# Kernel optimization log

Measured on AMD Instinct MI355X. Metric: run time of the kernel, lower is better.

Reference implementation:

```python
import jax, jax.numpy as jnp
import numpy as np

RATIO = 0.5
BN_EPS = 1e-5
L2_EPS = 1e-8


def setup_inputs() -> dict:
    key = jax.random.key(0)
    ks = jax.random.split(key, 8)
    B, L, D, E = 64, 577, 512, 1024
    H = E // 2  # MLP hidden = embed_dim // 2 = 512
    base_features = jax.random.normal(ks[0], (B, L, D), dtype=jnp.float32)
    atten = jax.random.uniform(ks[1], (B, L, L), dtype=jnp.float32)
    s_fc = 1.0 / np.sqrt(D)
    s_h = 1.0 / np.sqrt(H)
    return {
        "base_features": base_features,
        "atten": atten,
        "fc_w": jax.random.uniform(ks[2], (E, D), jnp.float32, -s_fc, s_fc),
        "fc_b": jax.random.uniform(ks[3], (E,), jnp.float32, -s_fc, s_fc),
        "mlp_w0": jax.random.uniform(ks[4], (H, D), jnp.float32, -s_fc, s_fc),
        "mlp_b0": jax.random.uniform(ks[5], (H,), jnp.float32, -s_fc, s_fc),
        "bn0_gamma": jnp.ones((H,), jnp.float32),
        "bn0_beta": jnp.zeros((H,), jnp.float32),
        "mlp_w1": jax.random.uniform(ks[6], (E, H), jnp.float32, -s_h, s_h),
        "mlp_b1": jax.random.uniform(ks[7], (E,), jnp.float32, -s_h, s_h),
    }


def _forward(base_features, atten, fc_w, fc_b, mlp_w0, mlp_b0,
             bn0_gamma, bn0_beta, mlp_w1, mlp_b1):
    B, L, D = base_features.shape
    k = int((L - 1) * RATIO)  # static: derived from shape

    # atten[:, :, 0] = -1; rank tokens by CLS-row attention atten[:, 0]
    scores = atten[:, 0].at[:, 0].set(-1.0)           # [B, L]
    idx = jax.lax.top_k(scores, k)[1]                 # [B, k]

    # gather selected tokens: [B, k, D]
    feats = jnp.take_along_axis(base_features, idx[:, :, None], axis=1)

    # l2norm over last dim (norm = sqrt(sum(x^2)) + eps, then divide)
    norm = jnp.sqrt(jnp.sum(feats * feats, axis=-1, keepdims=True)) + L2_EPS
    feats = feats / norm

    # MLP (num_layers=2): Linear -> BN(training-mode batch stats) -> ReLU -> Linear
    x = feats.reshape(B * k, D)
    h = x @ mlp_w0.T + mlp_b0                         # [B*k, H]
    mu = jnp.mean(h, axis=0)
    var = jnp.mean((h - mu) ** 2, axis=0)             # biased var, as torch BN
    h = jax.nn.relu(bn0_gamma * (h - mu) * jax.lax.rsqrt(var + BN_EPS) + bn0_beta)
    x_att = (h @ mlp_w1.T + mlp_b1).reshape(B, k, -1)  # [B, k, E]

    local = jnp.einsum('bkd,ed->bke', feats, fc_w) + fc_b + x_att

    # maxk_pool1d_var with k=1 and full lengths == max over sequence dim
    return jnp.max(local, axis=1).astype(jnp.float32)  # [B, E]


def reference(base_features, atten, fc_w, fc_b, mlp_w0, mlp_b0,
              bn0_gamma, bn0_beta, mlp_w1, mlp_b1):
    return _forward(base_features, atten, fc_w, fc_b, mlp_w0, mlp_b0,
                    bn0_gamma, bn0_beta, mlp_w1, mlp_b1)
```

## Files before the change

### kernel.cpp

```cpp
#include <hip/hip_runtime.h>
#include <math.h>

#define B_   64
#define L_   577
#define D_   512
#define E_   1024
#define H_   512
#define K_   288
#define N_   (B_ * K_)
#define KBIG 1024

typedef __attribute__((ext_vector_type(8))) __bf16 bf16x8;
typedef __attribute__((ext_vector_type(4))) float f32x4;
typedef __attribute__((ext_vector_type(4))) unsigned short ushort4v;

#define OFF_WBIG    0
#define OFF_W0B     (2097152)
#define OFF_BIASBIG (2097152 + 524288)
#define OFF_MUSIG   (OFF_BIASBIG + 4096)
#define OFF_IDX     (OFF_MUSIG + 4096)
#define OFF_PART    (OFF_IDX + 73728)
#define OFF_ABIG    (OFF_PART + 524288)
#define OFF_H       (OFF_ABIG + (size_t)N_ * KBIG * 2)
#define OFF_LOCAL   (OFF_H + (size_t)N_ * H_ * 4)

static __device__ __forceinline__ unsigned short f2bf(float f) {
  unsigned int u = __builtin_bit_cast(unsigned int, f);
  u = (u + 0x7fffu + ((u >> 16) & 1u)) >> 16;
  return (unsigned short)u;
}

#define GLOAD_LDS16(g, l)                                          \
  __builtin_amdgcn_global_load_lds(                                \
      (const __attribute__((address_space(1))) void*)(g),          \
      (__attribute__((address_space(3))) void*)(l), 16, 0, 0)

__global__ __launch_bounds__(256) void prep_kernel(
    const float* __restrict__ fc_w, const float* __restrict__ fc_b,
    const float* __restrict__ w0,   const float* __restrict__ w1,
    const float* __restrict__ b1,
    unsigned short* __restrict__ wbig, unsigned short* __restrict__ w0b,
    float* __restrict__ biasbig) {
  int gid = blockIdx.x * 256 + threadIdx.x;
  if (gid < 262144) {
    int e  = gid >> 8;
    int c4 = gid & 255;
    float4 v;
    if (c4 < 128) v = ((const float4*)(fc_w + e * D_))[c4];
    else          v = ((const float4*)(w1   + e * H_))[c4 - 128];
    ushort4v o = { f2bf(v.x), f2bf(v.y), f2bf(v.z), f2bf(v.w) };
    ((ushort4v*)wbig)[gid] = o;
    if (gid < E_) biasbig[gid] = fc_b[gid] + b1[gid];
  } else {
    int idx = gid - 262144;
    float4 v = ((const float4*)w0)[idx];
    ushort4v o = { f2bf(v.x), f2bf(v.y), f2bf(v.z), f2bf(v.w) };
    ((ushort4v*)w0b)[idx] = o;
  }
}

__global__ __launch_bounds__(256) void topk_kernel(
    const float* __restrict__ atten, int* __restrict__ idx) {
  __shared__ float s[L_];
  int b = blockIdx.x;
  const float* row = atten + (size_t)b * L_ * L_;
  for (int i = threadIdx.x; i < L_; i += 256) s[i] = (i == 0) ? -1.0f : row[i];
  __syncthreads();
  for (int i = threadIdx.x; i < L_; i += 256) {
    float si = s[i];
    int rank = 0;
    for (int j = 0; j < L_; ++j) {
      float sj = s[j];
      rank += (sj > si) || (sj == si && j < i);
    }
    if (rank < K_) idx[b * K_ + rank] = i;
  }
}

__global__ __launch_bounds__(128) void gather_norm_kernel(
    const float* __restrict__ base, const int* __restrict__ idx,
    unsigned short* __restrict__ abig) {
  int r = blockIdx.x;
  int b = r / K_;
  int tok = idx[r];
  const float* src = base + ((size_t)b * L_ + tok) * D_;
  float4 v = ((const float4*)src)[threadIdx.x];
  float ss = v.x * v.x + v.y * v.y + v.z * v.z + v.w * v.w;
  #pragma unroll
  for (int o = 32; o > 0; o >>= 1) ss += __shfl_down(ss, o, 64);
  __shared__ float wsum[2];
  if ((threadIdx.x & 63) == 0) wsum[threadIdx.x >> 6] = ss;
  __syncthreads();
  float total = wsum[0] + wsum[1];
  float inv = 1.0f / (sqrtf(total) + 1e-8f);
  ushort4v o4 = { f2bf(v.x * inv), f2bf(v.y * inv), f2bf(v.z * inv), f2bf(v.w * inv) };
  ((ushort4v*)(abig + (size_t)r * KBIG))[threadIdx.x] = o4;
}

__global__ __launch_bounds__(256) void gemm_mfma_kernel(
    const unsigned short* __restrict__ A, int lda,
    const unsigned short* __restrict__ W, int ldw,
    const float* __restrict__ bias,
    float* __restrict__ C, int ldc, int K) {
  __shared__ unsigned short As[128 * 32];
  __shared__ unsigned short Bs[128 * 32];
  const int tid  = threadIdx.x;
  const int wave = tid >> 6;
  const int lane = tid & 63;
  const int m0 = blockIdx.x * 128;
  const int n0 = blockIdx.y * 128;

  const int srow0 = 16 * wave + (lane >> 2);
  const int srow1 = srow0 + 64;
  const int scol  = (lane & 3) * 8;
  const unsigned short* ag0 = A + (size_t)(m0 + srow0) * lda + scol;
  const unsigned short* ag1 = A + (size_t)(m0 + srow1) * lda + scol;
  const unsigned short* wg0 = W + (size_t)(n0 + srow0) * ldw + scol;
  const unsigned short* wg1 = W + (size_t)(n0 + srow1) * ldw + scol;
  unsigned short* as_dst0 = &As[srow0 * 32 + scol];
  unsigned short* as_dst1 = &As[srow1 * 32 + scol];
  unsigned short* bs_dst0 = &Bs[srow0 * 32 + scol];
  unsigned short* bs_dst1 = &Bs[srow1 * 32 + scol];

  const int quad = lane >> 4;
  const int l15  = lane & 15;
  const int wm = (wave & 1) * 64;
  const int wn = (wave >> 1) * 64;

  f32x4 acc[4][4];
  #pragma unroll
  for (int i = 0; i < 4; ++i)
    #pragma unroll
    for (int j = 0; j < 4; ++j)
      acc[i][j] = (f32x4)(0.0f);

  for (int k0 = 0; k0 < K; k0 += 32) {
    GLOAD_LDS16(ag0 + k0, as_dst0);
    GLOAD_LDS16(ag1 + k0, as_dst1);
    GLOAD_LDS16(wg0 + k0, bs_dst0);
    GLOAD_LDS16(wg1 + k0, bs_dst1);
    __syncthreads();
    bf16x8 af[4], bfr[4];
    #pragma unroll
    for (int i = 0; i < 4; ++i)
      af[i] = *(const bf16x8*)&As[(wm + 16 * i + l15) * 32 + quad * 8];
    #pragma unroll
    for (int j = 0; j < 4; ++j)
      bfr[j] = *(const bf16x8*)&Bs[(wn + 16 * j + l15) * 32 + quad * 8];
    #pragma unroll
    for (int i = 0; i < 4; ++i)
      #pragma unroll
      for (int j = 0; j < 4; ++j)
        acc[i][j] = __builtin_amdgcn_mfma_f32_16x16x32_bf16(af[i], bfr[j], acc[i][j], 0, 0, 0);
    __syncthreads();
  }

  #pragma unroll
  for (int i = 0; i < 4; ++i) {
    int row_base = m0 + wm + 16 * i + quad * 4;
    #pragma unroll
    for (int j = 0; j < 4; ++j) {
      int col = n0 + wn + 16 * j + l15;
      float bb = bias[col];
      #pragma unroll
      for (int r = 0; r < 4; ++r)
        C[(size_t)(row_base + r) * ldc + col] = acc[i][j][r] + bb;
    }
  }
}

__global__ __launch_bounds__(256) void bn_stats1_kernel(
    const float* __restrict__ h, float* __restrict__ partial) {
  int blk = blockIdx.x;
  int t = threadIdx.x;
  int r0 = blk * 144;
  float s0 = 0.f, q0 = 0.f, s1 = 0.f, q1 = 0.f;
  for (int i = 0; i < 144; ++i) {
    const float* row = h + (size_t)(r0 + i) * H_;
    float a = row[t], b2 = row[t + 256];
    s0 += a; q0 += a * a; s1 += b2; q1 += b2 * b2;
  }
  partial[blk * 512 + t] = s0;
  partial[blk * 512 + t + 256] = s1;
  partial[65536 + blk * 512 + t] = q0;
  partial[65536 + blk * 512 + t + 256] = q1;
}

__global__ __launch_bounds__(256) void bn_stats2_kernel(
    const float* __restrict__ partial, float* __restrict__ musig) {
  int c = blockIdx.x * 256 + threadIdx.x;
  float S = 0.f, Q = 0.f;
  for (int i = 0; i < 128; ++i) {
    S += partial[i * 512 + c];
    Q += partial[65536 + i * 512 + c];
  }
  const float invN = 1.0f / (float)N_;
  float mu = S * invN;
  float var = Q * invN - mu * mu;
  musig[c] = mu;
  musig[512 + c] = rsqrtf(var + 1e-5f);
}

__global__ __launch_bounds__(256) void bn_apply_kernel(
    const float* __restrict__ h, unsigned short* __restrict__ abig,
    const float* __restrict__ musig,
    const float* __restrict__ gamma, const float* __restrict__ beta) {
  int gid = blockIdx.x * 256 + threadIdx.x;
  int r = gid >> 7;
  int c4 = gid & 127;
  int c = c4 * 4;
  float4 v = *((const float4*)(h + (size_t)r * H_) + c4);
  float vv[4] = {v.x, v.y, v.z, v.w};
  unsigned short o[4];
  #pragma unroll
  for (int j = 0; j < 4; ++j) {
    float x = (vv[j] - musig[c + j]) * musig[512 + c + j] * gamma[c + j] + beta[c + j];
    o[j] = f2bf(fmaxf(x, 0.0f));
  }
  ushort4v ov = { o[0], o[1], o[2], o[3] };
  *((ushort4v*)(abig + (size_t)r * KBIG + H_) + c4) = ov;
}

__global__ __launch_bounds__(256) void maxk_kernel(
    const float* __restrict__ local, float* __restrict__ out) {
  int gid = blockIdx.x * 256 + threadIdx.x;
  int b = gid >> 10, e = gid & 1023;
  const float* p = local + (size_t)b * K_ * KBIG + e;
  float m = -INFINITY;
  for (int j = 0; j < K_; ++j) m = fmaxf(m, p[(size_t)j * KBIG]);
  out[gid] = m;
}

extern "C" void kernel_launch(void* const* d_in, const int* in_sizes, int n_in,
                              void* d_out, int out_size, void* d_ws, size_t ws_size,
                              hipStream_t stream) {
  const float* base  = (const float*)d_in[0];
  const float* atten = (const float*)d_in[1];
  const float* fc_w  = (const float*)d_in[2];
  const float* fc_b  = (const float*)d_in[3];
  const float* w0    = (const float*)d_in[4];
  const float* b0    = (const float*)d_in[5];
  const float* gamma = (const float*)d_in[6];
  const float* beta  = (const float*)d_in[7];
  const float* w1    = (const float*)d_in[8];
  const float* b1    = (const float*)d_in[9];
  float* out = (float*)d_out;

  char* ws = (char*)d_ws;
  unsigned short* wbig    = (unsigned short*)(ws + OFF_WBIG);
  unsigned short* w0b     = (unsigned short*)(ws + OFF_W0B);
  float*          biasbig = (float*)(ws + OFF_BIASBIG);
  float*          musig   = (float*)(ws + OFF_MUSIG);
  int*            idx     = (int*)  (ws + OFF_IDX);
  float*          partial = (float*)(ws + OFF_PART);
  unsigned short* abig    = (unsigned short*)(ws + OFF_ABIG);
  float*          h       = (float*)(ws + OFF_H);
  float*          local   = (float*)(ws + OFF_LOCAL);

  prep_kernel<<<1280, 256, 0, stream>>>(fc_w, fc_b, w0, w1, b1, wbig, w0b, biasbig);
  topk_kernel<<<B_, 256, 0, stream>>>(atten, idx);
  gather_norm_kernel<<<N_, 128, 0, stream>>>(base, idx, abig);
  {
    dim3 grid(N_ / 128, H_ / 128);
    gemm_mfma_kernel<<<grid, 256, 0, stream>>>(abig, KBIG, w0b, D_, b0, h, H_, D_);
  }
  bn_stats1_kernel<<<128, 256, 0, stream>>>(h, partial);
  bn_stats2_kernel<<<2, 256, 0, stream>>>(partial, musig);
  bn_apply_kernel<<<(N_ * 128) / 256, 256, 0, stream>>>(h, abig, musig, gamma, beta);
  {
    dim3 grid(N_ / 128, E_ / 128);
    gemm_mfma_kernel<<<grid, 256, 0, stream>>>(abig, KBIG, wbig, KBIG, biasbig,
                                               local, KBIG, KBIG);
  }
  maxk_kernel<<<(B_ * E_) / 256, 256, 0, stream>>>(local, out);
}
```

Measured before the change: 355.9 us.

## Fuse BN stats and max-pool into GEMM epilogues, swizzle LDS tiles

The first GEMM's epilogue now computes per-tile column sums and sums of squares, which removes the separate BN statistics pass over h. The second GEMM reduces each output tile to a per-batch column max and merges it into an order-preserving encoded uint buffer with atomicMax. This removes the 75MB local intermediate and the maxk kernel. An XOR swizzle on the LDS column layout is also added to reduce bank conflicts on fragment reads. The costs are atomics, a zero-init step in prep and a small decode kernel.

```diff
diff --git a/kernel.cpp b/kernel.cpp
--- a/kernel.cpp
+++ b/kernel.cpp
@@ -9,25 +9,36 @@
 #define K_   288
 #define N_   (B_ * K_)
 #define KBIG 1024
+#define MTILES (N_ / 128)
 
 typedef __attribute__((ext_vector_type(8))) __bf16 bf16x8;
 typedef __attribute__((ext_vector_type(4))) float f32x4;
 typedef __attribute__((ext_vector_type(4))) unsigned short ushort4v;
 
 #define OFF_WBIG    0
-#define OFF_W0B     (2097152)
-#define OFF_BIASBIG (2097152 + 524288)
-#define OFF_MUSIG   (OFF_BIASBIG + 4096)
-#define OFF_IDX     (OFF_MUSIG + 4096)
-#define OFF_PART    (OFF_IDX + 73728)
-#define OFF_ABIG    (OFF_PART + 524288)
-#define OFF_H       (OFF_ABIG + (size_t)N_ * KBIG * 2)
-#define OFF_LOCAL   (OFF_H + (size_t)N_ * H_ * 4)
+#define OFF_W0B     2097152
+#define OFF_BIASBIG 2621440
+#define OFF_MUSIG   2625536
+#define OFF_IDX     2629632
+#define OFF_PSUM    2703360
+#define OFF_PSQ     2998272
+#define OFF_OUTENC  3293184
+#define OFF_ABIG    3555328
+#define OFF_H       (3555328 + (size_t)N_ * KBIG * 2)
 
 static __device__ __forceinline__ unsigned short f2bf(float f) {
   unsigned int u = __builtin_bit_cast(unsigned int, f);
   u = (u + 0x7fffu + ((u >> 16) & 1u)) >> 16;
   return (unsigned short)u;
+}
+
+static __device__ __forceinline__ unsigned int encf(float f) {
+  unsigned int u = __builtin_bit_cast(unsigned int, f);
+  return (u & 0x80000000u) ? ~u : (u | 0x80000000u);
+}
+static __device__ __forceinline__ float decf(unsigned int e) {
+  unsigned int u = (e & 0x80000000u) ? (e ^ 0x80000000u) : ~e;
+  return __builtin_bit_cast(float, u);
 }
 
 #define GLOAD_LDS16(g, l)                                          \
@@ -40,8 +51,9 @@
     const float* __restrict__ w0,   const float* __restrict__ w1,
     const float* __restrict__ b1,
     unsigned short* __restrict__ wbig, unsigned short* __restrict__ w0b,
-    float* __restrict__ biasbig) {
+    float* __restrict__ biasbig, unsigned int* __restrict__ outenc) {
   int gid = blockIdx.x * 256 + threadIdx.x;
+  if (gid < 65536) outenc[gid] = 0u;
   if (gid < 262144) {
     int e  = gid >> 8;
     int c4 = gid & 255;
@@ -97,13 +109,18 @@
   ((ushort4v*)(abig + (size_t)r * KBIG))[threadIdx.x] = o4;
 }
 
+template <int MODE>
 __global__ __launch_bounds__(256) void gemm_mfma_kernel(
     const unsigned short* __restrict__ A, int lda,
     const unsigned short* __restrict__ W, int ldw,
     const float* __restrict__ bias,
-    float* __restrict__ C, int ldc, int K) {
+    float* __restrict__ C, int ldc, int K,
+    float* __restrict__ psum, float* __restrict__ psq,
+    unsigned int* __restrict__ outenc) {
   __shared__ unsigned short As[128 * 32];
   __shared__ unsigned short Bs[128 * 32];
+  __shared__ float s_sum[4][64];
+  __shared__ float s_sq[4][64];
   const int tid  = threadIdx.x;
   const int wave = tid >> 6;
   const int lane = tid & 63;
@@ -112,20 +129,22 @@
 
   const int srow0 = 16 * wave + (lane >> 2);
   const int srow1 = srow0 + 64;
-  const int scol  = (lane & 3) * 8;
-  const unsigned short* ag0 = A + (size_t)(m0 + srow0) * lda + scol;
-  const unsigned short* ag1 = A + (size_t)(m0 + srow1) * lda + scol;
-  const unsigned short* wg0 = W + (size_t)(n0 + srow0) * ldw + scol;
-  const unsigned short* wg1 = W + (size_t)(n0 + srow1) * ldw + scol;
-  unsigned short* as_dst0 = &As[srow0 * 32 + scol];
-  unsigned short* as_dst1 = &As[srow1 * 32 + scol];
-  unsigned short* bs_dst0 = &Bs[srow0 * 32 + scol];
-  unsigned short* bs_dst1 = &Bs[srow1 * 32 + scol];
+  const int gcol  = (((lane & 3) ^ ((lane >> 3) & 3))) * 8;
+  const int lcol  = (lane & 3) * 8;
+  const unsigned short* ag0 = A + (size_t)(m0 + srow0) * lda + gcol;
+  const unsigned short* ag1 = A + (size_t)(m0 + srow1) * lda + gcol;
+  const unsigned short* wg0 = W + (size_t)(n0 + srow0) * ldw + gcol;
+  const unsigned short* wg1 = W + (size_t)(n0 + srow1) * ldw + gcol;
+  unsigned short* as_dst0 = &As[srow0 * 32 + lcol];
+  unsigned short* as_dst1 = &As[srow1 * 32 + lcol];
+  unsigned short* bs_dst0 = &Bs[srow0 * 32 + lcol];
+  unsigned short* bs_dst1 = &Bs[srow1 * 32 + lcol];
 
   const int quad = lane >> 4;
   const int l15  = lane & 15;
   const int wm = (wave & 1) * 64;
   const int wn = (wave >> 1) * 64;
+  const int rswz = (l15 >> 1) & 3;
 
   f32x4 acc[4][4];
   #pragma unroll
@@ -143,10 +162,10 @@
     bf16x8 af[4], bfr[4];
     #pragma unroll
     for (int i = 0; i < 4; ++i)
-      af[i] = *(const bf16x8*)&As[(wm + 16 * i + l15) * 32 + quad * 8];
+      af[i] = *(const bf16x8*)&As[(wm + 16 * i + l15) * 32 + (quad ^ rswz) * 8];
     #pragma unroll
     for (int j = 0; j < 4; ++j)
-      bfr[j] = *(const bf16x8*)&Bs[(wn + 16 * j + l15) * 32 + quad * 8];
+      bfr[j] = *(const bf16x8*)&Bs[(wn + 16 * j + l15) * 32 + (quad ^ rswz) * 8];
     #pragma unroll
     for (int i = 0; i < 4; ++i)
       #pragma unroll
@@ -155,44 +174,77 @@
     __syncthreads();
   }
 
-  #pragma unroll
-  for (int i = 0; i < 4; ++i) {
-    int row_base = m0 + wm + 16 * i + quad * 4;
+  if (MODE == 0) {
     #pragma unroll
     for (int j = 0; j < 4; ++j) {
       int col = n0 + wn + 16 * j + l15;
       float bb = bias[col];
+      float sm = 0.f, sq = 0.f;
       #pragma unroll
-      for (int r = 0; r < 4; ++r)
-        C[(size_t)(row_base + r) * ldc + col] = acc[i][j][r] + bb;
+      for (int i = 0; i < 4; ++i) {
+        int row_base = m0 + wm + 16 * i + quad * 4;
+        #pragma unroll
+        for (int r = 0; r < 4; ++r) {
+          float v = acc[i][j][r] + bb;
+          C[(size_t)(row_base + r) * ldc + col] = v;
+          sm += v; sq += v * v;
+        }
+      }
+      sm += __shfl_xor(sm, 16, 64); sm += __shfl_xor(sm, 32, 64);
+      sq += __shfl_xor(sq, 16, 64); sq += __shfl_xor(sq, 32, 64);
+      if (quad == 0) { s_sum[wave][j * 16 + l15] = sm; s_sq[wave][j * 16 + l15] = sq; }
     }
-  }
-}
-
-__global__ __launch_bounds__(256) void bn_stats1_kernel(
-    const float* __restrict__ h, float* __restrict__ partial) {
-  int blk = blockIdx.x;
-  int t = threadIdx.x;
-  int r0 = blk * 144;
-  float s0 = 0.f, q0 = 0.f, s1 = 0.f, q1 = 0.f;
-  for (int i = 0; i < 144; ++i) {
-    const float* row = h + (size_t)(r0 + i) * H_;
-    float a = row[t], b2 = row[t + 256];
-    s0 += a; q0 += a * a; s1 += b2; q1 += b2 * b2;
-  }
-  partial[blk * 512 + t] = s0;
-  partial[blk * 512 + t + 256] = s1;
-  partial[65536 + blk * 512 + t] = q0;
-  partial[65536 + blk * 512 + t + 256] = q1;
+    __syncthreads();
+    if (tid < 128) {
+      int half = tid >> 6;
+      int c = tid & 63;
+      float sm = s_sum[half * 2][c] + s_sum[half * 2 + 1][c];
+      float sq = s_sq[half * 2][c] + s_sq[half * 2 + 1][c];
+      int col = n0 + half * 64 + c;
+      psum[blockIdx.x * H_ + col] = sm;
+      psq [blockIdx.x * H_ + col] = sq;
+    }
+  } else {
+    #pragma unroll
+    for (int j = 0; j < 4; ++j) {
+      int col = n0 + wn + 16 * j + l15;
+      float bb = bias[col];
+      float m[4];
+      #pragma unroll
+      for (int i = 0; i < 4; ++i) {
+        float v = fmaxf(fmaxf(acc[i][j][0], acc[i][j][1]),
+                        fmaxf(acc[i][j][2], acc[i][j][3]));
+        m[i] = v + bb;
+      }
+      #pragma unroll
+      for (int i = 0; i < 4; ++i) {
+        m[i] = fmaxf(m[i], __shfl_xor(m[i], 16, 64));
+        m[i] = fmaxf(m[i], __shfl_xor(m[i], 32, 64));
+      }
+      if (quad == 0) {
+        int base = m0 + wm;
+        int b0i = (base) / K_;
+        float cur = m[0]; int cb = b0i;
+        #pragma unroll
+        for (int i = 1; i < 4; ++i) {
+          int bi = (base + 16 * i) / K_;
+          if (bi == cb) cur = fmaxf(cur, m[i]);
+          else { atomicMax(&outenc[cb * E_ + col], encf(cur)); cur = m[i]; cb = bi; }
+        }
+        atomicMax(&outenc[cb * E_ + col], encf(cur));
+      }
+    }
+  }
 }
 
 __global__ __launch_bounds__(256) void bn_stats2_kernel(
-    const float* __restrict__ partial, float* __restrict__ musig) {
+    const float* __restrict__ psum, const float* __restrict__ psq,
+    float* __restrict__ musig) {
   int c = blockIdx.x * 256 + threadIdx.x;
   float S = 0.f, Q = 0.f;
-  for (int i = 0; i < 128; ++i) {
-    S += partial[i * 512 + c];
-    Q += partial[65536 + i * 512 + c];
+  for (int mx = 0; mx < MTILES; ++mx) {
+    S += psum[mx * H_ + c];
+    Q += psq [mx * H_ + c];
   }
   const float invN = 1.0f / (float)N_;
   float mu = S * invN;
@@ -221,14 +273,10 @@
   *((ushort4v*)(abig + (size_t)r * KBIG + H_) + c4) = ov;
 }
 
-__global__ __launch_bounds__(256) void maxk_kernel(
-    const float* __restrict__ local, float* __restrict__ out) {
+__global__ __launch_bounds__(256) void decode_kernel(
+    const unsigned int* __restrict__ outenc, float* __restrict__ out) {
   int gid = blockIdx.x * 256 + threadIdx.x;
-  int b = gid >> 10, e = gid & 1023;
-  const float* p = local + (size_t)b * K_ * KBIG + e;
-  float m = -INFINITY;
-  for (int j = 0; j < K_; ++j) m = fmaxf(m, p[(size_t)j * KBIG]);
-  out[gid] = m;
+  out[gid] = decf(outenc[gid]);
 }
 
 extern "C" void kernel_launch(void* const* d_in, const int* in_sizes, int n_in,
@@ -252,25 +300,28 @@
   float*          biasbig = (float*)(ws + OFF_BIASBIG);
   float*          musig   = (float*)(ws + OFF_MUSIG);
   int*            idx     = (int*)  (ws + OFF_IDX);
-  float*          partial = (float*)(ws + OFF_PART);
+  float*          psum    = (float*)(ws + OFF_PSUM);
+  float*          psq     = (float*)(ws + OFF_PSQ);
+  unsigned int*   outenc  = (unsigned int*)(ws + OFF_OUTENC);
   unsigned short* abig    = (unsigned short*)(ws + OFF_ABIG);
   float*          h       = (float*)(ws + OFF_H);
-  float*          local   = (float*)(ws + OFF_LOCAL);
-
-  prep_kernel<<<1280, 256, 0, stream>>>(fc_w, fc_b, w0, w1, b1, wbig, w0b, biasbig);
+
+  prep_kernel<<<1280, 256, 0, stream>>>(fc_w, fc_b, w0, w1, b1, wbig, w0b,
+                                        biasbig, outenc);
   topk_kernel<<<B_, 256, 0, stream>>>(atten, idx);
   gather_norm_kernel<<<N_, 128, 0, stream>>>(base, idx, abig);
   {
-    dim3 grid(N_ / 128, H_ / 128);
-    gemm_mfma_kernel<<<grid, 256, 0, stream>>>(abig, KBIG, w0b, D_, b0, h, H_, D_);
-  }
-  bn_stats1_kernel<<<128, 256, 0, stream>>>(h, partial);
-  bn_stats2_kernel<<<2, 256, 0, stream>>>(partial, musig);
+    dim3 grid(MTILES, H_ / 128);
+    gemm_mfma_kernel<0><<<grid, 256, 0, stream>>>(abig, KBIG, w0b, D_, b0,
+                                                  h, H_, D_, psum, psq, nullptr);
+  }
+  bn_stats2_kernel<<<2, 256, 0, stream>>>(psum, psq, musig);
   bn_apply_kernel<<<(N_ * 128) / 256, 256, 0, stream>>>(h, abig, musig, gamma, beta);
   {
-    dim3 grid(N_ / 128, E_ / 128);
-    gemm_mfma_kernel<<<grid, 256, 0, stream>>>(abig, KBIG, wbig, KBIG, biasbig,
-                                               local, KBIG, KBIG);
-  }
-  maxk_kernel<<<(B_ * E_) / 256, 256, 0, stream>>>(local, out);
-}
+    dim3 grid(MTILES, E_ / 128);
+    gemm_mfma_kernel<1><<<grid, 256, 0, stream>>>(abig, KBIG, wbig, KBIG, biasbig,
+                                                  nullptr, 0, KBIG, nullptr, nullptr,
+                                                  outenc);
+  }
+  decode_kernel<<<(B_ * E_) / 256, 256, 0, stream>>>(outenc, out);
+}
```

Result: faster. 318.2 us (-10.6%).
